# Performance work log

Hardware: AMD Instinct MI355X
Metric: run time of the kernel (lower is better)

Reference implementation:

```python
import jax, jax.numpy as jnp
import numpy as np

N_HEAD = 12

def setup_inputs() -> dict:
    key = jax.random.key(0)
    ks = jax.random.split(key, 5)
    B, T, C = 4, 2048, 768
    scale = 0.02
    return {
        "x": jax.random.normal(ks[0], (B, T, C), dtype=jnp.float32),
        "W_attn": jax.random.normal(ks[1], (C, 3 * C), dtype=jnp.float32) * scale,
        "b_attn": jax.random.normal(ks[2], (3 * C,), dtype=jnp.float32) * scale,
        "W_proj": jax.random.normal(ks[3], (C, C), dtype=jnp.float32) * scale,
        "b_proj": jax.random.normal(ks[4], (C,), dtype=jnp.float32) * scale,
    }

def reference(x, W_attn, b_attn, W_proj, b_proj):
    B, T, C = x.shape
    H = N_HEAD
    D = C // H  # head dim
    qkv = x @ W_attn + b_attn  # [B,T,3C]
    q, k, v = jnp.split(qkv, 3, axis=-1)
    # [B,H,T,D]
    q = q.reshape(B, T, H, D).transpose(0, 2, 1, 3)
    k = k.reshape(B, T, H, D).transpose(0, 2, 1, 3)
    v = v.reshape(B, T, H, D).transpose(0, 2, 1, 3)
    scores = jnp.einsum('bhqd,bhkd->bhqk', q, k) / jnp.sqrt(jnp.float32(D))
    causal = jnp.tril(jnp.ones((T, T), dtype=bool))
    scores = jnp.where(causal[None, None, :, :], scores, jnp.float32(-jnp.inf))
    attn = jax.nn.softmax(scores, axis=-1)
    out = jnp.einsum('bhqk,bhkd->bhqd', attn, v)  # [B,H,T,D]
    out = out.transpose(0, 2, 1, 3).reshape(B, T, C)
    return out @ W_proj + b_proj
```

## Files before the change

kernel.cpp:

```cpp
#include <hip/hip_runtime.h>

typedef float f32x4 __attribute__((ext_vector_type(4)));
typedef __bf16 bf16x8 __attribute__((ext_vector_type(8)));
typedef unsigned short u16x8 __attribute__((ext_vector_type(8)));
typedef unsigned short u16x4 __attribute__((ext_vector_type(4)));

#define MFMA16(a, b, c) __builtin_amdgcn_mfma_f32_16x16x32_bf16((a), (b), (c), 0, 0, 0)

__device__ __forceinline__ unsigned short f2bf(float f) {
    __bf16 h = (__bf16)f;
    union { __bf16 h; unsigned short u; } c; c.h = h;
    return c.u;
}

__device__ __forceinline__ void gload_lds16(const unsigned short* g, unsigned short* l) {
    __builtin_amdgcn_global_load_lds(
        (const __attribute__((address_space(1))) unsigned int*)g,
        (__attribute__((address_space(3))) unsigned int*)l, 16, 0, 0);
}

__global__ void k_convert_bf16(const float* __restrict__ in,
                               unsigned short* __restrict__ out, int n) {
    int i = (blockIdx.x * 256 + threadIdx.x) * 4;
    if (i + 3 < n) {
        float4 v = *reinterpret_cast<const float4*>(in + i);
        ushort4 o;
        o.x = f2bf(v.x); o.y = f2bf(v.y); o.z = f2bf(v.z); o.w = f2bf(v.w);
        *reinterpret_cast<ushort4*>(out + i) = o;
    }
}

__global__ void k_transpose_bf16(const float* __restrict__ in,
                                 unsigned short* __restrict__ out, int R, int C) {
    __shared__ unsigned short tile[32][33];
    int bx = blockIdx.x * 32;
    int by = blockIdx.y * 32;
    int tx = threadIdx.x;
    int ty = threadIdx.y;
    #pragma unroll
    for (int i = ty; i < 32; i += 8)
        tile[i][tx] = f2bf(in[(size_t)(by + i) * C + bx + tx]);
    __syncthreads();
    #pragma unroll
    for (int i = ty; i < 32; i += 8)
        out[(size_t)(bx + i) * R + by + tx] = tile[tx][i];
}

__global__ __launch_bounds__(512) void k_gemm_qkv(
    const unsigned short* __restrict__ A,
    const unsigned short* __restrict__ Bt,
    const float* __restrict__ bias,
    unsigned short* __restrict__ Qo,
    unsigned short* __restrict__ Ko,
    unsigned short* __restrict__ Vto,
    int K)
{
    __shared__ unsigned short SM[3 * 8192 + 3 * 4096];
    const int nwg = gridDim.x * gridDim.y;
    const int bid0 = blockIdx.y * gridDim.x + blockIdx.x;
    const int logical = (bid0 & 7) * (nwg >> 3) + (bid0 >> 3);
    const int bm = logical / gridDim.x;
    const int bn = logical % gridDim.x;
    const int tid = threadIdx.x;
    const int w = tid >> 6, l = tid & 63;
    const int wm = w >> 1, wn = w & 1;
    const int ln = l & 15, kb = l >> 4;

    f32x4 acc[4][4];
    #pragma unroll
    for (int i = 0; i < 4; ++i)
        #pragma unroll
        for (int j = 0; j < 4; ++j)
            #pragma unroll
            for (int r = 0; r < 4; ++r) acc[i][j][r] = 0.f;

    const unsigned short* Ab = A + (size_t)(bm * 256) * K;
    const unsigned short* Bb = Bt + (size_t)(bn * 128) * K;

    const int srow = tid >> 2;
    const int sslot = tid & 3;
    const int scs = (sslot ^ ((srow >> 1) & 3)) * 8;
    const int slot8 = (kb ^ ((ln >> 1) & 3)) * 8;
    const int aOff = (wm * 64 + ln) * 32 + slot8;
    const int bOff = 24576 + (wn * 64 + ln) * 32 + slot8;

    #define QSTAGE(t_, buf_)                                                        \
        {                                                                           \
            const int k0_ = (t_) * 32;                                              \
            gload_lds16(&Ab[(size_t)srow * K + k0_ + scs],                          \
                        &SM[(buf_) * 8192 + srow * 32 + sslot * 8]);                \
            gload_lds16(&Ab[(size_t)(128 + srow) * K + k0_ + scs],                  \
                        &SM[(buf_) * 8192 + (128 + srow) * 32 + sslot * 8]);        \
            gload_lds16(&Bb[(size_t)srow * K + k0_ + scs],                          \
                        &SM[24576 + (buf_) * 4096 + srow * 32 + sslot * 8]);        \
        }

    #define QSTEP(t_, BUF_, NBUF_)                                                  \
        {                                                                           \
            if ((t_) < 23) { asm volatile("s_waitcnt vmcnt(3)" ::: "memory"); }     \
            else           { asm volatile("s_waitcnt vmcnt(0)" ::: "memory"); }     \
            __builtin_amdgcn_sched_barrier(0);                                      \
            __builtin_amdgcn_s_barrier();                                           \
            if ((t_) + 2 < 24) QSTAGE((t_) + 2, NBUF_);                             \
            bf16x8 af[4], bfr[4];                                                   \
            _Pragma("unroll")                                                       \
            for (int mt = 0; mt < 4; ++mt)                                          \
                af[mt] = *reinterpret_cast<const bf16x8*>(                          \
                    &SM[(BUF_) * 8192 + mt * 512 + aOff]);                          \
            _Pragma("unroll")                                                       \
            for (int nt = 0; nt < 4; ++nt)                                          \
                bfr[nt] = *reinterpret_cast<const bf16x8*>(                         \
                    &SM[(BUF_) * 4096 + nt * 512 + bOff]);                          \
            _Pragma("unroll")                                                       \
            for (int mt = 0; mt < 4; ++mt)                                          \
                _Pragma("unroll")                                                   \
                for (int nt = 0; nt < 4; ++nt)                                      \
                    acc[mt][nt] = MFMA16(af[mt], bfr[nt], acc[mt][nt]);             \
        }

    QSTAGE(0, 0);
    QSTAGE(1, 1);
    #pragma unroll
    for (int s = 0; s < 8; ++s) {
        QSTEP(3 * s,     0, 2);
        QSTEP(3 * s + 1, 1, 0);
        QSTEP(3 * s + 2, 2, 1);
    }
    __syncthreads();

    const float SC = 0.1803368801111204f;

    if (bn >= 12) {
        unsigned short* Ts = SM;
        const int cl_w = wn * 64;
        #pragma unroll
        for (int hh2 = 0; hh2 < 2; ++hh2) {
            if ((wm >> 1) == hh2) {
                #pragma unroll
                for (int mt = 0; mt < 4; ++mt) {
                    #pragma unroll
                    for (int nt = 0; nt < 4; ++nt) {
                        const int cl = cl_w + nt * 16 + ln;
                        const float bv = bias[bn * 128 + cl];
                        #pragma unroll
                        for (int r = 0; r < 4; ++r) {
                            const int rl = (wm & 1) * 64 + mt * 16 + kb * 4 + r;
                            const int pos = cl * 128 + ((((rl >> 3) ^ (cl & 7)) << 3) | (rl & 7));
                            Ts[pos] = f2bf(acc[mt][nt][r] + bv);
                        }
                    }
                }
            }
            __syncthreads();
            {
                const int cl = tid >> 2;
                const int col = bn * 128 + cl;
                const int cc = col - 1536;
                const int hh = cc >> 6, dd = cc & 63;
                #pragma unroll
                for (int j8 = 0; j8 < 4; ++j8) {
                    const int rb = (tid & 3) * 4 + j8;
                    u16x8 val = *reinterpret_cast<const u16x8*>(&Ts[cl * 128 + ((rb ^ (cl & 7)) << 3)]);
                    const int tg = bm * 256 + hh2 * 128 + rb * 8;
                    const int bb = tg >> 11;
                    const int tloc = tg & 2047;
                    const int grp = tloc & ~31;
                    const int jj = (tloc >> 3) & 3;
                    const int tlo = grp + 8 * ((2 * jj) & 3) + 4 * (jj >> 1);
                    const int thi = grp + 8 * ((2 * jj + 1) & 3) + 4 * (jj >> 1);
                    unsigned short* basep = &Vto[((size_t)((bb * 12 + hh) * 64 + dd)) * 2048];
                    *reinterpret_cast<u16x4*>(basep + tlo) =
                        __builtin_shufflevector(val, val, 0, 1, 2, 3);
                    *reinterpret_cast<u16x4*>(basep + thi) =
                        __builtin_shufflevector(val, val, 4, 5, 6, 7);
                }
            }
            __syncthreads();
        }
        return;
    }

    #pragma unroll
    for (int mt = 0; mt < 4; ++mt) {
        #pragma unroll
        for (int nt = 0; nt < 4; ++nt) {
            const int col = bn * 128 + wn * 64 + nt * 16 + ln;
            #pragma unroll
            for (int r = 0; r < 4; ++r) {
                const int row = bm * 256 + wm * 64 + mt * 16 + kb * 4 + r;
                float v = acc[mt][nt][r] + bias[col];
                int cc = col >= 768 ? col - 768 : col;
                int h = cc >> 6, d = cc & 63;
                int b = row >> 11, t = row & 2047;
                if (col < 768)
                    Qo[((size_t)((b * 12 + h) * 2048 + t)) * 64 + d] = f2bf(v * SC);
                else
                    Ko[((size_t)((b * 12 + h) * 2048 + t)) * 64 + d] = f2bf(v);
            }
        }
    }
    #undef QSTAGE
    #undef QSTEP
}

__global__ __launch_bounds__(256) void k_gemm_proj(
    const unsigned short* __restrict__ A,
    const unsigned short* __restrict__ Bt,
    const float* __restrict__ bias,
    float* __restrict__ Co,
    int K)
{
    constexpr int BM = 128;
    __shared__ unsigned short SM[(BM + 128) * 64];
    unsigned short* As = SM;
    unsigned short* Bs = SM + BM * 64;
    const int nwg = gridDim.x * gridDim.y;
    const int bid0 = blockIdx.y * gridDim.x + blockIdx.x;
    const int logical = (bid0 & 7) * (nwg >> 3) + (bid0 >> 3);
    const int bm = logical / gridDim.x;
    const int bn = logical % gridDim.x;
    const int tid = threadIdx.x;
    const int w = tid >> 6, l = tid & 63;
    const int wm = w >> 1, wn = w & 1;
    const int ln = l & 15, kb = l >> 4;

    f32x4 acc[4][4];
    #pragma unroll
    for (int i = 0; i < 4; ++i)
        #pragma unroll
        for (int j = 0; j < 4; ++j)
            #pragma unroll
            for (int r = 0; r < 4; ++r) acc[i][j][r] = 0.f;

    const unsigned short* Ab = A + (size_t)(bm * BM) * K;
    const unsigned short* Bb = Bt + (size_t)(bn * 128) * K;

    const int srow = tid >> 3;
    const int sslot = tid & 7;
    const int csw = (sslot ^ (srow & 7)) * 8;

    for (int k0 = 0; k0 < K; k0 += 64) {
        #pragma unroll
        for (int j = 0; j < 4; ++j) {
            const int r = j * 32 + srow;
            gload_lds16(&Ab[(size_t)r * K + k0 + csw], &As[r * 64 + sslot * 8]);
        }
        #pragma unroll
        for (int j = 0; j < 4; ++j) {
            const int r = j * 32 + srow;
            gload_lds16(&Bb[(size_t)r * K + k0 + csw], &Bs[r * 64 + sslot * 8]);
        }
        __syncthreads();
        #pragma unroll
        for (int kh = 0; kh < 2; ++kh) {
            bf16x8 af[4], bfr[4];
            #pragma unroll
            for (int mt = 0; mt < 4; ++mt) {
                const int row = wm * 64 + mt * 16 + ln;
                const int slot = ((kh << 2) | kb) ^ (row & 7);
                af[mt] = *reinterpret_cast<const bf16x8*>(&As[row * 64 + slot * 8]);
            }
            #pragma unroll
            for (int nt = 0; nt < 4; ++nt) {
                const int row = wn * 64 + nt * 16 + ln;
                const int slot = ((kh << 2) | kb) ^ (row & 7);
                bfr[nt] = *reinterpret_cast<const bf16x8*>(&Bs[row * 64 + slot * 8]);
            }
            #pragma unroll
            for (int mt = 0; mt < 4; ++mt)
                #pragma unroll
                for (int nt = 0; nt < 4; ++nt)
                    acc[mt][nt] = MFMA16(af[mt], bfr[nt], acc[mt][nt]);
        }
        __syncthreads();
    }

    #pragma unroll
    for (int mt = 0; mt < 4; ++mt) {
        #pragma unroll
        for (int nt = 0; nt < 4; ++nt) {
            const int col = bn * 128 + wn * 64 + nt * 16 + ln;
            #pragma unroll
            for (int r = 0; r < 4; ++r) {
                const int row = bm * BM + wm * 64 + mt * 16 + kb * 4 + r;
                Co[(size_t)row * 768 + col] = acc[mt][nt][r] + bias[col];
            }
        }
    }
}

__global__ __launch_bounds__(256) void k_attn(
    const unsigned short* __restrict__ Q,
    const unsigned short* __restrict__ Kk,
    const unsigned short* __restrict__ Vt,
    unsigned short* __restrict__ Oo)
{
    __shared__ unsigned short SMEM[4 * 4096];
    const int bid0 = blockIdx.x;
    const int xcd = bid0 & 7;
    const int loc = bid0 >> 3;
    const int qb = 15 - (loc / 6);
    const int bh = xcd * 6 + (loc % 6);
    const int tid = threadIdx.x;
    const int w = tid >> 6, l = tid & 63;
    const int ln = l & 15, kb = l >> 4;
    const int kbq = kb * 4;
    const int b = bh / 12, h = bh - b * 12;
    const int q0w = qb * 128 + w * 32;

    const unsigned short* Qb = Q + (size_t)bh * 2048 * 64;
    const unsigned short* Kb = Kk + (size_t)bh * 2048 * 64;
    const unsigned short* Vb = Vt + (size_t)bh * 64 * 2048;

    bf16x8 qf[2][2];
    #pragma unroll
    for (int qn = 0; qn < 2; ++qn) {
        const unsigned short* qr = &Qb[(size_t)(q0w + qn * 16 + ln) * 64 + kb * 8];
        qf[qn][0] = *reinterpret_cast<const bf16x8*>(qr);
        qf[qn][1] = *reinterpret_cast<const bf16x8*>(qr + 32);
    }

    bf16x8 vones;
    #pragma unroll
    for (int e = 0; e < 8; ++e) vones[e] = (__bf16)1.0f;
    const f32x4 fzero = {0.f, 0.f, 0.f, 0.f};

    f32x4 oaccT[2][4];
    f32x4 den[2];
    #pragma unroll
    for (int qn = 0; qn < 2; ++qn) {
        #pragma unroll
        for (int r = 0; r < 4; ++r) den[qn][r] = 0.f;
        #pragma unroll
        for (int dt = 0; dt < 4; ++dt)
            #pragma unroll
            for (int r = 0; r < 4; ++r) oaccT[qn][dt][r] = 0.f;
    }

    const int lb = ln & 7;
    const int aR0 = ln * 64 + (kb ^ lb) * 8;
    const int aR1 = ln * 64 + ((4 | kb) ^ lb) * 8;

    const int srow = tid >> 3;
    const int sslot = tid & 7;
    const int csw = (sslot ^ (srow & 7)) * 8;
    const int lastkt = (q0w + 31) >> 6;

    #define STAGE(kt_, buf_)                                                        \
        {                                                                           \
            const int kb_ = (kt_) * 64;                                             \
            _Pragma("unroll")                                                       \
            for (int j = 0; j < 2; ++j) {                                           \
                const int r = j * 32 + srow;                                        \
                gload_lds16(&Kb[(size_t)(kb_ + r) * 64 + csw],                      \
                            &SMEM[(buf_) * 4096 + r * 64 + sslot * 8]);             \
                gload_lds16(&Vb[(size_t)r * 2048 + kb_ + csw],                      \
                            &SMEM[8192 + (buf_) * 4096 + r * 64 + sslot * 8]);      \
            }                                                                       \
        }

    #define COMPUTE(kt_, BUF)                                                       \
        if ((kt_) <= lastkt) {                                                      \
            bf16x8 kf[4][2];                                                        \
            _Pragma("unroll")                                                       \
            for (int km = 0; km < 4; ++km) {                                        \
                kf[km][0] = *reinterpret_cast<const bf16x8*>(                       \
                    &SMEM[(BUF) * 4096 + km * 1024 + aR0]);                         \
                kf[km][1] = *reinterpret_cast<const bf16x8*>(                       \
                    &SMEM[(BUF) * 4096 + km * 1024 + aR1]);                         \
            }                                                                       \
            f32x4 st[4][2];                                                         \
            _Pragma("unroll")                                                       \
            for (int km = 0; km < 4; ++km)                                          \
                _Pragma("unroll")                                                   \
                for (int qn = 0; qn < 2; ++qn) {                                    \
                    st[km][qn] = MFMA16(kf[km][0], qf[qn][0], fzero);               \
                    st[km][qn] = MFMA16(kf[km][1], qf[qn][1], st[km][qn]);          \
                }                                                                   \
            bf16x8 vf[4][2];                                                        \
            _Pragma("unroll")                                                       \
            for (int dt = 0; dt < 4; ++dt) {                                        \
                vf[dt][0] = *reinterpret_cast<const bf16x8*>(                       \
                    &SMEM[8192 + (BUF) * 4096 + dt * 1024 + aR0]);                  \
                vf[dt][1] = *reinterpret_cast<const bf16x8*>(                       \
                    &SMEM[8192 + (BUF) * 4096 + dt * 1024 + aR1]);                  \
            }                                                                       \
            if ((kt_) == lastkt) {                                                  \
                const int kbase_ = (kt_) * 64;                                      \
                _Pragma("unroll")                                                   \
                for (int qn = 0; qn < 2; ++qn) {                                    \
                    const int qrow = q0w + qn * 16 + ln;                            \
                    _Pragma("unroll")                                               \
                    for (int km = 0; km < 4; ++km)                                  \
                        _Pragma("unroll")                                           \
                        for (int r = 0; r < 4; ++r) {                               \
                            float sv = st[km][qn][r];                               \
                            const int key = kbase_ + km * 16 + kbq + r;             \
                            sv = (key <= qrow) ? sv : -1e30f;                       \
                            st[km][qn][r] = __builtin_amdgcn_exp2f(sv);             \
                        }                                                           \
                }                                                                   \
            } else {                                                                \
                _Pragma("unroll")                                                   \
                for (int qn = 0; qn < 2; ++qn)                                      \
                    _Pragma("unroll")                                               \
                    for (int km = 0; km < 4; ++km)                                  \
                        _Pragma("unroll")                                           \
                        for (int r = 0; r < 4; ++r)                                 \
                            st[km][qn][r] =                                         \
                                __builtin_amdgcn_exp2f(st[km][qn][r]);              \
            }                                                                       \
            bf16x8 pa[2][2];                                                        \
            _Pragma("unroll")                                                       \
            for (int qn = 0; qn < 2; ++qn)                                          \
                _Pragma("unroll")                                                   \
                for (int kh = 0; kh < 2; ++kh) {                                    \
                    bf16x8 t;                                                       \
                    _Pragma("unroll")                                               \
                    for (int r = 0; r < 4; ++r) {                                   \
                        t[r]     = (__bf16)st[2 * kh][qn][r];                       \
                        t[r + 4] = (__bf16)st[2 * kh + 1][qn][r];                   \
                    }                                                               \
                    pa[qn][kh] = t;                                                 \
                }                                                                   \
            _Pragma("unroll")                                                       \
            for (int qn = 0; qn < 2; ++qn) {                                        \
                _Pragma("unroll")                                                   \
                for (int dt = 0; dt < 4; ++dt) {                                    \
                    oaccT[qn][dt] = MFMA16(pa[qn][0], vf[dt][0], oaccT[qn][dt]);    \
                    oaccT[qn][dt] = MFMA16(pa[qn][1], vf[dt][1], oaccT[qn][dt]);    \
                }                                                                   \
                den[qn] = MFMA16(pa[qn][0], vones, den[qn]);                        \
                den[qn] = MFMA16(pa[qn][1], vones, den[qn]);                        \
            }                                                                       \
        }

    STAGE(0, 0);

    for (int s = 0; s <= qb; ++s) {
        const int ktA = 2 * s;
        const int ktB = 2 * s + 1;
        __syncthreads();
        STAGE(ktB, 1);
        COMPUTE(ktA, 0);
        __syncthreads();
        if (s < qb) STAGE(ktA + 2, 0);
        COMPUTE(ktB, 1);
    }

    #pragma unroll
    for (int qn = 0; qn < 2; ++qn) {
        #pragma unroll
        for (int r = 0; r < 4; ++r) {
            const float inv = 1.0f / den[qn][r];
            const int t = q0w + qn * 16 + kbq + r;
            #pragma unroll
            for (int dt = 0; dt < 4; ++dt)
                Oo[((size_t)(b * 2048 + t)) * 768 + h * 64 + dt * 16 + ln] =
                    f2bf(oaccT[qn][dt][r] * inv);
        }
    }
    #undef STAGE
    #undef COMPUTE
}

extern "C" void kernel_launch(void* const* d_in, const int* in_sizes, int n_in,
                              void* d_out, int out_size, void* d_ws, size_t ws_size,
                              hipStream_t stream) {
    const float* x      = (const float*)d_in[0];
    const float* W_attn = (const float*)d_in[1];
    const float* b_attn = (const float*)d_in[2];
    const float* W_proj = (const float*)d_in[3];
    const float* b_proj = (const float*)d_in[4];
    float* out = (float*)d_out;

    char* ws = (char*)d_ws;
    const size_t SZ_X  = (size_t)8192 * 768 * 2;
    const size_t SZ_WA = (size_t)2304 * 768 * 2;
    const size_t SZ_WP = (size_t)768 * 768 * 2;
    const size_t SZ_T  = (size_t)8192 * 768 * 2;

    unsigned short* x_bf = (unsigned short*)(ws);
    unsigned short* wa_t = (unsigned short*)(ws + SZ_X);
    unsigned short* wp_t = (unsigned short*)(ws + SZ_X + SZ_WA);
    unsigned short* Qb   = (unsigned short*)(ws + SZ_X + SZ_WA + SZ_WP);
    unsigned short* Kb   = (unsigned short*)(ws + SZ_X + SZ_WA + SZ_WP + SZ_T);
    unsigned short* Vtb  = (unsigned short*)(ws + SZ_X + SZ_WA + SZ_WP + 2 * SZ_T);
    unsigned short* attn_o = x_bf;

    k_convert_bf16<<<6144, 256, 0, stream>>>(x, x_bf, 8192 * 768);
    dim3 tb(32, 8);
    k_transpose_bf16<<<dim3(2304 / 32, 768 / 32), tb, 0, stream>>>(W_attn, wa_t, 768, 2304);
    k_transpose_bf16<<<dim3(768 / 32, 768 / 32), tb, 0, stream>>>(W_proj, wp_t, 768, 768);
    k_gemm_qkv<<<dim3(18, 32), 512, 0, stream>>>(x_bf, wa_t, b_attn, Qb, Kb, Vtb, 768);
    k_attn<<<768, 256, 0, stream>>>(Qb, Kb, Vtb, attn_o);
    k_gemm_proj<<<dim3(6, 64), 256, 0, stream>>>(attn_o, wp_t, b_proj, out, 768);
}
```

Measured before the change: 117.5 us.

## Restructure QKV GEMM to double-buffered BK=64 pipeline with 8-slot swizzle

Replaces the QKV GEMM's triple-buffered K=32 pipeline, which used fine-grained vmcnt waits and raw barriers, with a double-buffered K=64 loop that uses __syncthreads per iteration. Each stage loads a 64-wide k slab with an XOR swizzle over 8 slots, and each iteration runs two MFMA sub-steps. The intent is to halve the number of barriers and loop iterations and to improve LDS access patterns. In exchange, only one stage is in flight, and the __syncthreads waits on all outstanding loads, so the prefetch overlap may weaken. LDS usage also rises from 72 KB to 96 KB per block.

```diff
diff --git a/kernel.cpp b/kernel.cpp
--- a/kernel.cpp
+++ b/kernel.cpp
@@ -55,7 +55,7 @@
     unsigned short* __restrict__ Vto,
     int K)
 {
-    __shared__ unsigned short SM[3 * 8192 + 3 * 4096];
+    __shared__ unsigned short SM[2 * 16384 + 2 * 8192];
     const int nwg = gridDim.x * gridDim.y;
     const int bid0 = blockIdx.y * gridDim.x + blockIdx.x;
     const int logical = (bid0 & 7) * (nwg >> 3) + (bid0 >> 3);
@@ -77,56 +77,58 @@
     const unsigned short* Ab = A + (size_t)(bm * 256) * K;
     const unsigned short* Bb = Bt + (size_t)(bn * 128) * K;
 
-    const int srow = tid >> 2;
-    const int sslot = tid & 3;
-    const int scs = (sslot ^ ((srow >> 1) & 3)) * 8;
-    const int slot8 = (kb ^ ((ln >> 1) & 3)) * 8;
-    const int aOff = (wm * 64 + ln) * 32 + slot8;
-    const int bOff = 24576 + (wn * 64 + ln) * 32 + slot8;
+    const int srow = tid >> 3;
+    const int sslot = tid & 7;
+    const int csw = (sslot ^ (srow & 7)) * 8;
 
     #define QSTAGE(t_, buf_)                                                        \
         {                                                                           \
-            const int k0_ = (t_) * 32;                                              \
-            gload_lds16(&Ab[(size_t)srow * K + k0_ + scs],                          \
-                        &SM[(buf_) * 8192 + srow * 32 + sslot * 8]);                \
-            gload_lds16(&Ab[(size_t)(128 + srow) * K + k0_ + scs],                  \
-                        &SM[(buf_) * 8192 + (128 + srow) * 32 + sslot * 8]);        \
-            gload_lds16(&Bb[(size_t)srow * K + k0_ + scs],                          \
-                        &SM[24576 + (buf_) * 4096 + srow * 32 + sslot * 8]);        \
-        }
-
-    #define QSTEP(t_, BUF_, NBUF_)                                                  \
-        {                                                                           \
-            if ((t_) < 23) { asm volatile("s_waitcnt vmcnt(3)" ::: "memory"); }     \
-            else           { asm volatile("s_waitcnt vmcnt(0)" ::: "memory"); }     \
-            __builtin_amdgcn_sched_barrier(0);                                      \
-            __builtin_amdgcn_s_barrier();                                           \
-            if ((t_) + 2 < 24) QSTAGE((t_) + 2, NBUF_);                             \
-            bf16x8 af[4], bfr[4];                                                   \
-            _Pragma("unroll")                                                       \
-            for (int mt = 0; mt < 4; ++mt)                                          \
-                af[mt] = *reinterpret_cast<const bf16x8*>(                          \
-                    &SM[(BUF_) * 8192 + mt * 512 + aOff]);                          \
-            _Pragma("unroll")                                                       \
-            for (int nt = 0; nt < 4; ++nt)                                          \
-                bfr[nt] = *reinterpret_cast<const bf16x8*>(                         \
-                    &SM[(BUF_) * 4096 + nt * 512 + bOff]);                          \
-            _Pragma("unroll")                                                       \
-            for (int mt = 0; mt < 4; ++mt)                                          \
-                _Pragma("unroll")                                                   \
-                for (int nt = 0; nt < 4; ++nt)                                      \
-                    acc[mt][nt] = MFMA16(af[mt], bfr[nt], acc[mt][nt]);             \
+            const int k0_ = (t_) * 64;                                              \
+            _Pragma("unroll")                                                       \
+            for (int j = 0; j < 4; ++j) {                                           \
+                const int r = j * 64 + srow;                                        \
+                gload_lds16(&Ab[(size_t)r * K + k0_ + csw],                         \
+                            &SM[(buf_) * 16384 + r * 64 + sslot * 8]);              \
+            }                                                                       \
+            _Pragma("unroll")                                                       \
+            for (int j = 0; j < 2; ++j) {                                           \
+                const int r = j * 64 + srow;                                        \
+                gload_lds16(&Bb[(size_t)r * K + k0_ + csw],                         \
+                            &SM[32768 + (buf_) * 8192 + r * 64 + sslot * 8]);       \
+            }                                                                       \
         }
 
     QSTAGE(0, 0);
-    QSTAGE(1, 1);
-    #pragma unroll
-    for (int s = 0; s < 8; ++s) {
-        QSTEP(3 * s,     0, 2);
-        QSTEP(3 * s + 1, 1, 0);
-        QSTEP(3 * s + 2, 2, 1);
-    }
     __syncthreads();
+
+    for (int t = 0; t < 12; ++t) {
+        const int buf = t & 1;
+        if (t + 1 < 12) QSTAGE(t + 1, buf ^ 1);
+        #pragma unroll
+        for (int kh = 0; kh < 2; ++kh) {
+            bf16x8 af[4], bfr[4];
+            #pragma unroll
+            for (int mt = 0; mt < 4; ++mt) {
+                const int row = wm * 64 + mt * 16 + ln;
+                const int slot = ((kh << 2) | kb) ^ (row & 7);
+                af[mt] = *reinterpret_cast<const bf16x8*>(
+                    &SM[buf * 16384 + row * 64 + slot * 8]);
+            }
+            #pragma unroll
+            for (int nt = 0; nt < 4; ++nt) {
+                const int row = wn * 64 + nt * 16 + ln;
+                const int slot = ((kh << 2) | kb) ^ (row & 7);
+                bfr[nt] = *reinterpret_cast<const bf16x8*>(
+                    &SM[32768 + buf * 8192 + row * 64 + slot * 8]);
+            }
+            #pragma unroll
+            for (int mt = 0; mt < 4; ++mt)
+                #pragma unroll
+                for (int nt = 0; nt < 4; ++nt)
+                    acc[mt][nt] = MFMA16(af[mt], bfr[nt], acc[mt][nt]);
+        }
+        __syncthreads();
+    }
 
     const float SC = 0.1803368801111204f;
 
@@ -200,7 +202,6 @@
         }
     }
     #undef QSTAGE
-    #undef QSTEP
 }
 
 __global__ __launch_bounds__(256) void k_gemm_proj(
```

Result: no change. 119.2 us (+1.4%).
